# Kernel tuning notes

Measured on AMD Instinct MI355X. Metric: run time of the kernel, lower is better.

The kernel has to match this reference:

```python
import jax, jax.numpy as jnp
import numpy as np

N_CLASSES = 64
TRANSDUCTIVE_STEPS = 5


def setup_inputs() -> dict:
    key = jax.random.key(0)
    k1, k2, k3, k4 = jax.random.split(key, 4)
    support = jax.random.normal(k1, (1280, 2048), dtype=jnp.float32)
    query = jax.random.normal(k2, (65536, 2048), dtype=jnp.float32)
    support_labels = jax.random.randint(k3, (1280,), 0, N_CLASSES)
    W_enc = jax.random.normal(k4, (2048, 1024), dtype=jnp.float32) * 0.02
    b_enc = jnp.zeros((1024,), dtype=jnp.float32)
    return {"support": support, "query": query, "support_labels": support_labels,
            "W_enc": W_enc, "b_enc": b_enc}


def _segment_mean(emb, labels, n_seg):
    # masked-mean per class; empty classes stay zero (sum=0 / 1)
    sums = jax.ops.segment_sum(emb, labels, num_segments=n_seg)
    counts = jax.ops.segment_sum(jnp.ones((emb.shape[0],), emb.dtype), labels,
                                 num_segments=n_seg)
    return sums / jnp.maximum(counts, 1.0)[:, None]


def _cdist(x, p):
    # euclidean distance [n, d] x [c, d] -> [n, c]
    d2 = (jnp.sum(x * x, -1)[:, None] + jnp.sum(p * p, -1)[None, :]
          - 2.0 * x @ p.T)
    return jnp.sqrt(jnp.maximum(d2, 1e-12))


def reference(support, query, support_labels, W_enc, b_enc):
    support_emb = support @ W_enc + b_enc   # [ns, d]
    query_emb = query @ W_enc + b_enc       # [nq, d]

    prototypes = _segment_mean(support_emb, support_labels, N_CLASSES)
    all_emb = jnp.concatenate([support_emb, query_emb], axis=0)
    for _ in range(TRANSDUCTIVE_STEPS):
        query_labels = jnp.argmin(_cdist(query_emb, prototypes), axis=-1)
        all_labels = jnp.concatenate([support_labels, query_labels], axis=0)
        prototypes = _segment_mean(all_emb, all_labels, N_CLASSES)

    logits = -_cdist(query_emb, prototypes)  # [nq, n_classes]
    return logits
```

## Files before the change

kernel.cpp:

```cpp
#include <hip/hip_runtime.h>
#include <hip/hip_bf16.h>

#define NS 1280
#define NQ 65536
#define NA (NS + NQ)
#define DIN 2048
#define DEMB 1024
#define NC 64
#define STEPS 5
#define NDBLK (NQ / 128)

typedef __attribute__((ext_vector_type(8))) __bf16 bf16x8;
typedef __attribute__((ext_vector_type(4))) float f32x4;
typedef unsigned short u16;

__device__ __forceinline__ float b2f(u16 u) {
  return __uint_as_float(((unsigned int)u) << 16);
}
__device__ __forceinline__ u16 f2b(float f) {
  __hip_bfloat16 h = __float2bfloat16(f);
  u16 u; __builtin_memcpy(&u, &h, 2); return u;
}
__device__ __forceinline__ void gld_lds16(const void* g, void* l) {
  __builtin_amdgcn_global_load_lds(
      (const __attribute__((address_space(1))) void*)g,
      (__attribute__((address_space(3))) void*)l, 16, 0, 0);
}

__global__ __launch_bounds__(256) void cvt_bf16(const float4* __restrict__ in,
                                                ushort4* __restrict__ out, int n4) {
  for (int i = blockIdx.x * 256 + threadIdx.x; i < n4; i += gridDim.x * 256) {
    float4 v = in[i];
    ushort4 o;
    o.x = f2b(v.x); o.y = f2b(v.y); o.z = f2b(v.z); o.w = f2b(v.w);
    out[i] = o;
  }
}

__global__ __launch_bounds__(256) void transpose_w(const float* __restrict__ W,
                                                   u16* __restrict__ Wt) {
  __shared__ float tile[32][33];
  const int bx = blockIdx.x;
  const int by = blockIdx.y;
  const int tx = threadIdx.x & 31, ty = threadIdx.x >> 5;
#pragma unroll
  for (int j = 0; j < 4; j++)
    tile[ty + 8 * j][tx] = W[(size_t)(by * 32 + ty + 8 * j) * DEMB + bx * 32 + tx];
  __syncthreads();
#pragma unroll
  for (int j = 0; j < 4; j++)
    Wt[(size_t)(bx * 32 + ty + 8 * j) * DIN + by * 32 + tx] = f2b(tile[tx][ty + 8 * j]);
}

__device__ __forceinline__ void mm16(const bf16x8 af[4], const bf16x8 bf[4],
                                     f32x4 (&acc)[4][4]) {
#pragma unroll
  for (int mt = 0; mt < 4; ++mt)
#pragma unroll
    for (int nt = 0; nt < 4; ++nt)
      acc[mt][nt] = __builtin_amdgcn_mfma_f32_16x16x32_bf16(af[mt], bf[nt],
                                                            acc[mt][nt], 0, 0, 0);
}

__global__ __launch_bounds__(512, 2) void encoder_gemm(const u16* __restrict__ A,
                                                       const u16* __restrict__ Bt,
                                                       const float* __restrict__ bias,
                                                       u16* __restrict__ C) {
  const int b = blockIdx.x;
  const int x = b & 7, tt = b >> 3;
  const int mblk = x + 8 * (tt >> 2);
  const int nblk = tt & 3;
  if (mblk >= NA / 256) return;

  __shared__ u16 lds[65536];

  const int m0 = mblk * 256, n0 = nblk * 256;
  const int t = threadIdx.x;
  const int w = t >> 6, l = t & 63;
  const int wm = (w >> 2) * 128;
  const int wn = (w & 3) * 64;
  const int lr = l & 15, lk8 = (l >> 4) * 8;
  const int swz = (lr & 7) << 3;

  const int c1 = t + 512;
  const int r0 = t >> 3, r1 = c1 >> 3;
  const int sc0 = (((t & 7) ^ (r0 & 7)) << 3);
  const int sc1 = (((c1 & 7) ^ (r1 & 7)) << 3);

  const u16* gAt = A + (size_t)m0 * DIN;
  const u16* gBt = Bt + (size_t)n0 * DIN;

  f32x4 acc[2][4][4];
  f32x4 z; z.x = 0.f; z.y = 0.f; z.z = 0.f; z.w = 0.f;
#pragma unroll
  for (int g = 0; g < 2; ++g)
#pragma unroll
    for (int i = 0; i < 4; ++i)
#pragma unroll
      for (int j = 0; j < 4; ++j) acc[g][i][j] = z;

  auto STAGE = [&](const u16* g, u16* S, int h, int kb) {
    gld_lds16(g + (size_t)(h * 128 + r0) * DIN + kb + sc0, S + h * 8192 + t * 8);
    gld_lds16(g + (size_t)(h * 128 + r1) * DIN + kb + sc1, S + h * 8192 + c1 * 8);
  };

  STAGE(gAt, lds, 0, 0);
  STAGE(gAt, lds, 1, 0);
  STAGE(gBt, lds + 16384, 0, 0);
  STAGE(gBt, lds + 16384, 1, 0);

  const int NT = DIN / 64;
  for (int tk = 0; tk < NT; ++tk) {
    const int p = tk & 1;
    u16* LA = lds + p * 32768;
    u16* LB = LA + 16384;
    u16* SA = lds + (p ^ 1) * 32768;
    u16* SB = SA + 16384;
    const int kbn = (tk + 1) * 64;
    const bool pre = (tk + 1 < NT);

    bf16x8 af[4], bf0[4], bf1[4];

    if (pre) {
      STAGE(gAt, SA, 0, kbn);
      asm volatile("s_waitcnt vmcnt(2)" ::: "memory");
    } else {
      asm volatile("s_waitcnt vmcnt(0)" ::: "memory");
    }
    __builtin_amdgcn_s_barrier();
#pragma unroll
    for (int mt = 0; mt < 4; ++mt)
      af[mt] = *(const bf16x8*)&LA[(wm + mt * 16 + lr) * 64 + (lk8 ^ swz)];
#pragma unroll
    for (int nt = 0; nt < 4; ++nt)
      bf0[nt] = *(const bf16x8*)&LB[(wn + nt * 16 + lr) * 64 + (lk8 ^ swz)];
    __builtin_amdgcn_s_setprio(1);
    mm16(af, bf0, acc[0]);
    __builtin_amdgcn_s_setprio(0);
    __builtin_amdgcn_s_barrier();

#pragma unroll
    for (int mt = 0; mt < 4; ++mt)
      af[mt] = *(const bf16x8*)&LA[(wm + 64 + mt * 16 + lr) * 64 + (lk8 ^ swz)];
    if (pre) STAGE(gAt, SA, 1, kbn);
    __builtin_amdgcn_s_barrier();
    __builtin_amdgcn_s_setprio(1);
    mm16(af, bf0, acc[1]);
    __builtin_amdgcn_s_setprio(0);
    __builtin_amdgcn_s_barrier();

#pragma unroll
    for (int mt = 0; mt < 4; ++mt)
      af[mt] = *(const bf16x8*)&LA[(wm + mt * 16 + lr) * 64 + ((32 + lk8) ^ swz)];
#pragma unroll
    for (int nt = 0; nt < 4; ++nt)
      bf1[nt] = *(const bf16x8*)&LB[(wn + nt * 16 + lr) * 64 + ((32 + lk8) ^ swz)];
    if (pre) STAGE(gBt, SB, 0, kbn);
    __builtin_amdgcn_s_barrier();
    __builtin_amdgcn_s_setprio(1);
    mm16(af, bf1, acc[0]);
    __builtin_amdgcn_s_setprio(0);
    __builtin_amdgcn_s_barrier();

#pragma unroll
    for (int mt = 0; mt < 4; ++mt)
      af[mt] = *(const bf16x8*)&LA[(wm + 64 + mt * 16 + lr) * 64 + ((32 + lk8) ^ swz)];
    if (pre) STAGE(gBt, SB, 1, kbn);
    __builtin_amdgcn_s_barrier();
    __builtin_amdgcn_s_setprio(1);
    mm16(af, bf1, acc[1]);
    __builtin_amdgcn_s_setprio(0);
    __builtin_amdgcn_s_barrier();
  }

  float bv[4];
#pragma unroll
  for (int nt = 0; nt < 4; ++nt) bv[nt] = bias[n0 + wn + nt * 16 + lr];
#pragma unroll
  for (int mg = 0; mg < 2; ++mg)
#pragma unroll
    for (int mt = 0; mt < 4; ++mt)
#pragma unroll
      for (int nt = 0; nt < 4; ++nt)
#pragma unroll
        for (int r = 0; r < 4; ++r) {
          int row = m0 + wm + mg * 64 + mt * 16 + (l >> 4) * 4 + r;
          int col = n0 + wn + nt * 16 + lr;
          C[(size_t)row * DEMB + col] = f2b(acc[mg][mt][nt][r] + bv[nt]);
        }
}

__global__ __launch_bounds__(256) void support_sums(const u16* __restrict__ emb,
                                                    const int* __restrict__ slab,
                                                    float* __restrict__ ssum,
                                                    int* __restrict__ scount) {
  const int c = blockIdx.x, t = threadIdx.x;
  __shared__ int lab[NS];
  for (int i = t; i < NS; i += 256) lab[i] = slab[i];
  __syncthreads();
  float a0 = 0, a1 = 0, a2 = 0, a3 = 0;
  int cnt = 0;
  for (int i = 0; i < NS; i++) {
    if (lab[i] == c) {
      ushort4 e = *(const ushort4*)&emb[(size_t)i * DEMB + t * 4];
      a0 += b2f(e.x); a1 += b2f(e.y); a2 += b2f(e.z); a3 += b2f(e.w);
      cnt++;
    }
  }
  float* dst = ssum + (size_t)c * DEMB + t * 4;
  dst[0] = a0; dst[1] = a1; dst[2] = a2; dst[3] = a3;
  if (t == 0) scount[c] = cnt;
}

__global__ __launch_bounds__(256) void qnorm_kernel(const u16* __restrict__ Q,
                                                    float* __restrict__ qnorm) {
  const int t = threadIdx.x, w = t >> 6, l = t & 63;
  const int row = blockIdx.x * 4 + w;
  const u16* p = Q + (size_t)row * DEMB;
  float s = 0.f;
#pragma unroll
  for (int kk = 0; kk < 4; kk++) {
    ushort4 e = *(const ushort4*)&p[kk * 256 + l * 4];
    float x0 = b2f(e.x), x1 = b2f(e.y), x2 = b2f(e.z), x3 = b2f(e.w);
    s += x0 * x0 + x1 * x1 + x2 * x2 + x3 * x3;
  }
#pragma unroll
  for (int d = 32; d >= 1; d >>= 1) s += __shfl_xor(s, d);
  if (l == 0) qnorm[row] = s;
}

template <bool INIT>
__global__ __launch_bounds__(256) void finalize_protos(const float* __restrict__ ssum,
                                                       const int* __restrict__ scount,
                                                       const float* __restrict__ qpart,
                                                       const int* __restrict__ histpart,
                                                       u16* __restrict__ protos,
                                                       float* __restrict__ pnorm) {
  const int c = blockIdx.x, t = threadIdx.x;
  __shared__ int wredi[4];
  __shared__ float wredf[4];
  __shared__ int cnt_sh;
  float inv;
  if (INIT) {
    inv = 1.0f / fmaxf((float)scount[c], 1.0f);
  } else {
    int p = histpart[(size_t)c * NDBLK + t] + histpart[(size_t)c * NDBLK + 256 + t];
#pragma unroll
    for (int d = 32; d >= 1; d >>= 1) p += __shfl_xor(p, d);
    if ((t & 63) == 0) wredi[t >> 6] = p;
    __syncthreads();
    if (t == 0) cnt_sh = scount[c] + wredi[0] + wredi[1] + wredi[2] + wredi[3];
    __syncthreads();
    inv = 1.0f / fmaxf((float)cnt_sh, 1.0f);
  }
  float part = 0.f;
#pragma unroll
  for (int j = 0; j < 4; j++) {
    const int d = t * 4 + j;
    float v = ssum[(size_t)c * DEMB + d];
    if (!INIT) {
#pragma unroll
      for (int ch = 0; ch < 8; ch++)
        v += qpart[((size_t)ch * NC + c) * DEMB + d];
    }
    v *= inv;
    u16 bits = f2b(v);
    protos[(size_t)c * DEMB + d] = bits;
    float vb = b2f(bits);
    part += vb * vb;
  }
#pragma unroll
  for (int d = 32; d >= 1; d >>= 1) part += __shfl_xor(part, d);
  if ((t & 63) == 0) wredf[t >> 6] = part;
  __syncthreads();
  if (t == 0) pnorm[c] = wredf[0] + wredf[1] + wredf[2] + wredf[3];
}

template <int MODE>
__global__ __launch_bounds__(256) void dist_kernel(const u16* __restrict__ Q,
                                                   const u16* __restrict__ P,
                                                   const float* __restrict__ pnorm,
                                                   const float* __restrict__ qnorm,
                                                   int* __restrict__ labels,
                                                   int* __restrict__ histpart,
                                                   float* __restrict__ out) {
  __shared__ u16 As[128 * 32];
  __shared__ u16 Bs[64 * 32];
  __shared__ int hist[NC];
  const int t = threadIdx.x;
  if (MODE == 0 && t < NC) hist[t] = 0;
  const int m0 = blockIdx.x * 128;
  const int w = t >> 6, l = t & 63;
  const int lr = l & 15, lk = (l >> 4) * 8;
  const int wm = w * 32;

  f32x4 acc[2][4];
  f32x4 z; z.x = 0.f; z.y = 0.f; z.z = 0.f; z.w = 0.f;
#pragma unroll
  for (int i = 0; i < 2; i++)
#pragma unroll
    for (int j = 0; j < 4; j++) acc[i][j] = z;

  const int rA0 = t >> 2, k8 = (t & 3) * 8;
  const u16* gA = Q + (size_t)(m0 + rA0) * DEMB + k8;
  const u16* gB = P + (size_t)rA0 * DEMB + k8;
  u16* lA = As + t * 8;
  u16* lB = Bs + t * 8;

  for (int kb = 0; kb < DEMB; kb += 32) {
    gld_lds16(gA + kb, lA);
    gld_lds16(gA + kb + (size_t)64 * DEMB, lA + 64 * 32);
    gld_lds16(gB + kb, lB);
    __syncthreads();
    bf16x8 af[2], bf[4];
#pragma unroll
    for (int mt = 0; mt < 2; mt++) af[mt] = *(const bf16x8*)&As[(wm + mt * 16 + lr) * 32 + lk];
#pragma unroll
    for (int nt = 0; nt < 4; nt++) bf[nt] = *(const bf16x8*)&Bs[(nt * 16 + lr) * 32 + lk];
#pragma unroll
    for (int mt = 0; mt < 2; mt++)
#pragma unroll
      for (int nt = 0; nt < 4; nt++)
        acc[mt][nt] = __builtin_amdgcn_mfma_f32_16x16x32_bf16(af[mt], bf[nt], acc[mt][nt], 0, 0, 0);
    __syncthreads();
  }

  if (MODE == 0) {
#pragma unroll
    for (int mt = 0; mt < 2; mt++)
#pragma unroll
      for (int r = 0; r < 4; r++) {
        float best = 3.402e38f; int bc = 0;
#pragma unroll
        for (int nt = 0; nt < 4; nt++) {
          int col = nt * 16 + lr;
          float v = pnorm[col] - 2.0f * acc[mt][nt][r];
          if (v < best) { best = v; bc = col; }
        }
#pragma unroll
        for (int s = 1; s < 16; s <<= 1) {
          float ov = __shfl_xor(best, s);
          int oc = __shfl_xor(bc, s);
          if (ov < best || (ov == best && oc < bc)) { best = ov; bc = oc; }
        }
        if (lr == 0) {
          int row = m0 + wm + mt * 16 + (l >> 4) * 4 + r;
          labels[row] = bc;
          atomicAdd(&hist[bc], 1);
        }
      }
    __syncthreads();
    if (t < NC) histpart[(size_t)t * NDBLK + blockIdx.x] = hist[t];
  } else {
#pragma unroll
    for (int mt = 0; mt < 2; mt++)
#pragma unroll
      for (int nt = 0; nt < 4; nt++)
#pragma unroll
        for (int r = 0; r < 4; r++) {
          int row = m0 + wm + mt * 16 + (l >> 4) * 4 + r;
          int col = nt * 16 + lr;
          float d2 = qnorm[row] + pnorm[col] - 2.0f * acc[mt][nt][r];
          out[(size_t)row * NC + col] = -sqrtf(fmaxf(d2, 1e-12f));
        }
  }
}

__global__ __launch_bounds__(256) void class_gather_sum(const u16* __restrict__ Q,
                                                        const int* __restrict__ labels,
                                                        float* __restrict__ qpart) {
  const int c = blockIdx.x >> 3;
  const int chunk = blockIdx.x & 7;
  const int base = chunk * (NQ / 8);
  const int t = threadIdx.x;
  __shared__ int list[NQ / 8];
  __shared__ int nmatch;
  if (t == 0) nmatch = 0;
  __syncthreads();
  for (int i = t; i < NQ / 8; i += 256) {
    if (labels[base + i] == c) {
      int p = atomicAdd(&nmatch, 1);
      list[p] = base + i;
    }
  }
  __syncthreads();
  const int cnt = nmatch;
  float a0 = 0, a1 = 0, a2 = 0, a3 = 0;
  for (int j = 0; j < cnt; j++) {
    int row = list[j];
    ushort4 e = *(const ushort4*)&Q[(size_t)row * DEMB + t * 4];
    a0 += b2f(e.x); a1 += b2f(e.y); a2 += b2f(e.z); a3 += b2f(e.w);
  }
  float* dst = qpart + ((size_t)chunk * NC + c) * DEMB + t * 4;
  dst[0] = a0; dst[1] = a1; dst[2] = a2; dst[3] = a3;
}

extern "C" void kernel_launch(void* const* d_in, const int* in_sizes, int n_in,
                              void* d_out, int out_size, void* d_ws, size_t ws_size,
                              hipStream_t stream) {
  const float* support = (const float*)d_in[0];
  const float* query   = (const float*)d_in[1];
  const int*   slab    = (const int*)d_in[2];
  const float* W       = (const float*)d_in[3];
  const float* bias    = (const float*)d_in[4];
  float* out = (float*)d_out;

  u16* Abf = (u16*)d_ws;
  u16* Wt  = Abf + (size_t)NA * DIN;
  u16* emb = Wt + (size_t)DEMB * DIN;
  float* ssum  = (float*)(emb + (size_t)NA * DEMB);
  float* pnorm = ssum + (size_t)NC * DEMB;
  float* qnorm = pnorm + NC;
  int* scount  = (int*)(qnorm + NQ);
  int* labels  = scount + NC;
  u16* protos  = (u16*)(labels + NQ);
  float* qpart = (float*)Abf;
  int* histpart = (int*)(qpart + (size_t)8 * NC * DEMB);

  const u16* Qemb = emb + (size_t)NS * DEMB;

  cvt_bf16<<<2048, 256, 0, stream>>>((const float4*)support, (ushort4*)Abf,
                                     NS * DIN / 4);
  cvt_bf16<<<8192, 256, 0, stream>>>((const float4*)query,
                                     (ushort4*)(Abf + (size_t)NS * DIN),
                                     NQ * DIN / 4);
  transpose_w<<<dim3(32, 64), 256, 0, stream>>>(W, Wt);

  encoder_gemm<<<8 * 33 * 4, 512, 0, stream>>>(Abf, Wt, bias, emb);

  support_sums<<<NC, 256, 0, stream>>>(emb, slab, ssum, scount);
  qnorm_kernel<<<NQ / 4, 256, 0, stream>>>(Qemb, qnorm);

  finalize_protos<true><<<NC, 256, 0, stream>>>(ssum, scount, qpart, histpart,
                                                protos, pnorm);

  for (int it = 0; it < STEPS; ++it) {
    dist_kernel<0><<<NDBLK, 256, 0, stream>>>(Qemb, protos, pnorm, nullptr,
                                              labels, histpart, nullptr);
    class_gather_sum<<<NC * 8, 256, 0, stream>>>(Qemb, labels, qpart);
    finalize_protos<false><<<NC, 256, 0, stream>>>(ssum, scount, qpart, histpart,
                                                   protos, pnorm);
  }

  dist_kernel<1><<<NDBLK, 256, 0, stream>>>(Qemb, protos, pnorm, qnorm,
                                            nullptr, nullptr, out);
}
```

Before: 1.440 ms.

## Double-buffer dist kernel with swizzled 64-wide K tiles and issue GEMM prefetch upfront

```diff
diff --git a/kernel.cpp b/kernel.cpp
--- a/kernel.cpp
+++ b/kernel.cpp
@@ -123,7 +123,10 @@
 
     if (pre) {
       STAGE(gAt, SA, 0, kbn);
-      asm volatile("s_waitcnt vmcnt(2)" ::: "memory");
+      STAGE(gAt, SA, 1, kbn);
+      STAGE(gBt, SB, 0, kbn);
+      STAGE(gBt, SB, 1, kbn);
+      asm volatile("s_waitcnt vmcnt(8)" ::: "memory");
     } else {
       asm volatile("s_waitcnt vmcnt(0)" ::: "memory");
     }
@@ -142,7 +145,6 @@
 #pragma unroll
     for (int mt = 0; mt < 4; ++mt)
       af[mt] = *(const bf16x8*)&LA[(wm + 64 + mt * 16 + lr) * 64 + (lk8 ^ swz)];
-    if (pre) STAGE(gAt, SA, 1, kbn);
     __builtin_amdgcn_s_barrier();
     __builtin_amdgcn_s_setprio(1);
     mm16(af, bf0, acc[1]);
@@ -155,7 +157,6 @@
 #pragma unroll
     for (int nt = 0; nt < 4; ++nt)
       bf1[nt] = *(const bf16x8*)&LB[(wn + nt * 16 + lr) * 64 + ((32 + lk8) ^ swz)];
-    if (pre) STAGE(gBt, SB, 0, kbn);
     __builtin_amdgcn_s_barrier();
     __builtin_amdgcn_s_setprio(1);
     mm16(af, bf1, acc[0]);
@@ -165,7 +166,6 @@
 #pragma unroll
     for (int mt = 0; mt < 4; ++mt)
       af[mt] = *(const bf16x8*)&LA[(wm + 64 + mt * 16 + lr) * 64 + ((32 + lk8) ^ swz)];
-    if (pre) STAGE(gBt, SB, 1, kbn);
     __builtin_amdgcn_s_barrier();
     __builtin_amdgcn_s_setprio(1);
     mm16(af, bf1, acc[1]);
@@ -284,15 +284,16 @@
                                                    int* __restrict__ labels,
                                                    int* __restrict__ histpart,
                                                    float* __restrict__ out) {
-  __shared__ u16 As[128 * 32];
-  __shared__ u16 Bs[64 * 32];
+  __shared__ __align__(16) u16 Ab[2][128 * 64];
+  __shared__ __align__(16) u16 Bb[2][64 * 64];
   __shared__ int hist[NC];
   const int t = threadIdx.x;
   if (MODE == 0 && t < NC) hist[t] = 0;
   const int m0 = blockIdx.x * 128;
   const int w = t >> 6, l = t & 63;
-  const int lr = l & 15, lk = (l >> 4) * 8;
+  const int lr = l & 15, lk8 = (l >> 4) * 8;
   const int wm = w * 32;
+  const int swz = (lr & 7) << 3;
 
   f32x4 acc[2][4];
   f32x4 z; z.x = 0.f; z.y = 0.f; z.z = 0.f; z.w = 0.f;
@@ -301,28 +302,59 @@
 #pragma unroll
     for (int j = 0; j < 4; j++) acc[i][j] = z;
 
-  const int rA0 = t >> 2, k8 = (t & 3) * 8;
-  const u16* gA = Q + (size_t)(m0 + rA0) * DEMB + k8;
-  const u16* gB = P + (size_t)rA0 * DEMB + k8;
-  u16* lA = As + t * 8;
-  u16* lB = Bs + t * 8;
-
-  for (int kb = 0; kb < DEMB; kb += 32) {
-    gld_lds16(gA + kb, lA);
-    gld_lds16(gA + kb + (size_t)64 * DEMB, lA + 64 * 32);
-    gld_lds16(gB + kb, lB);
-    __syncthreads();
-    bf16x8 af[2], bf[4];
-#pragma unroll
-    for (int mt = 0; mt < 2; mt++) af[mt] = *(const bf16x8*)&As[(wm + mt * 16 + lr) * 32 + lk];
-#pragma unroll
-    for (int nt = 0; nt < 4; nt++) bf[nt] = *(const bf16x8*)&Bs[(nt * 16 + lr) * 32 + lk];
-#pragma unroll
-    for (int mt = 0; mt < 2; mt++)
-#pragma unroll
-      for (int nt = 0; nt < 4; nt++)
-        acc[mt][nt] = __builtin_amdgcn_mfma_f32_16x16x32_bf16(af[mt], bf[nt], acc[mt][nt], 0, 0, 0);
-    __syncthreads();
+  int rA[4], sA[4], rB[2], sB[2];
+#pragma unroll
+  for (int j = 0; j < 4; ++j) {
+    int c = t + 256 * j;
+    rA[j] = c >> 3;
+    sA[j] = ((c & 7) ^ (rA[j] & 7)) << 3;
+  }
+#pragma unroll
+  for (int j = 0; j < 2; ++j) {
+    int c = t + 256 * j;
+    rB[j] = c >> 3;
+    sB[j] = ((c & 7) ^ (rB[j] & 7)) << 3;
+  }
+
+  auto STAGE = [&](int buf, int kb) {
+#pragma unroll
+    for (int j = 0; j < 4; ++j)
+      gld_lds16(Q + (size_t)(m0 + rA[j]) * DEMB + kb + sA[j], &Ab[buf][(t + 256 * j) * 8]);
+#pragma unroll
+    for (int j = 0; j < 2; ++j)
+      gld_lds16(P + (size_t)rB[j] * DEMB + kb + sB[j], &Bb[buf][(t + 256 * j) * 8]);
+  };
+
+  STAGE(0, 0);
+  const int NT = DEMB / 64;
+  for (int tk = 0; tk < NT; ++tk) {
+    const int cur = tk & 1;
+    if (tk + 1 < NT) {
+      STAGE(cur ^ 1, (tk + 1) * 64);
+      asm volatile("s_waitcnt vmcnt(6)" ::: "memory");
+    } else {
+      asm volatile("s_waitcnt vmcnt(0)" ::: "memory");
+    }
+    __builtin_amdgcn_s_barrier();
+    bf16x8 af[2][2], bf[2][4];
+#pragma unroll
+    for (int kk = 0; kk < 2; ++kk) {
+#pragma unroll
+      for (int mt = 0; mt < 2; ++mt)
+        af[kk][mt] = *(const bf16x8*)&Ab[cur][(wm + mt * 16 + lr) * 64 + ((kk * 32 + lk8) ^ swz)];
+#pragma unroll
+      for (int nt = 0; nt < 4; ++nt)
+        bf[kk][nt] = *(const bf16x8*)&Bb[cur][(nt * 16 + lr) * 64 + ((kk * 32 + lk8) ^ swz)];
+    }
+#pragma unroll
+    for (int kk = 0; kk < 2; ++kk)
+#pragma unroll
+      for (int mt = 0; mt < 2; ++mt)
+#pragma unroll
+        for (int nt = 0; nt < 4; ++nt)
+          acc[mt][nt] = __builtin_amdgcn_mfma_f32_16x16x32_bf16(af[kk][mt], bf[kk][nt],
+                                                                acc[mt][nt], 0, 0, 0);
+    __builtin_amdgcn_s_barrier();
   }
 
   if (MODE == 0) {
```

Measured after the change: 1.513 ms. +5.0%, slower.

## Rework GEMM prefetch schedule and make dist kernel load operands directly from global

Applied to the files above, without the earlier changes.

```diff
diff --git a/kernel.cpp b/kernel.cpp
--- a/kernel.cpp
+++ b/kernel.cpp
@@ -8,7 +8,7 @@
 #define DEMB 1024
 #define NC 64
 #define STEPS 5
-#define NDBLK (NQ / 128)
+#define NDBLK (NQ / 64)
 
 typedef __attribute__((ext_vector_type(8))) __bf16 bf16x8;
 typedef __attribute__((ext_vector_type(4))) float f32x4;
@@ -108,6 +108,8 @@
   STAGE(gAt, lds, 1, 0);
   STAGE(gBt, lds + 16384, 0, 0);
   STAGE(gBt, lds + 16384, 1, 0);
+  asm volatile("s_waitcnt vmcnt(0)" ::: "memory");
+  __builtin_amdgcn_s_barrier();
 
   const int NT = DIN / 64;
   for (int tk = 0; tk < NT; ++tk) {
@@ -121,29 +123,28 @@
 
     bf16x8 af[4], bf0[4], bf1[4];
 
-    if (pre) {
-      STAGE(gAt, SA, 0, kbn);
-      asm volatile("s_waitcnt vmcnt(2)" ::: "memory");
-    } else {
-      asm volatile("s_waitcnt vmcnt(0)" ::: "memory");
-    }
-    __builtin_amdgcn_s_barrier();
+    if (pre) { STAGE(gAt, SA, 0, kbn); STAGE(gAt, SA, 1, kbn); }
 #pragma unroll
     for (int mt = 0; mt < 4; ++mt)
       af[mt] = *(const bf16x8*)&LA[(wm + mt * 16 + lr) * 64 + (lk8 ^ swz)];
 #pragma unroll
     for (int nt = 0; nt < 4; ++nt)
       bf0[nt] = *(const bf16x8*)&LB[(wn + nt * 16 + lr) * 64 + (lk8 ^ swz)];
+    __builtin_amdgcn_s_barrier();
+    asm volatile("s_waitcnt lgkmcnt(0)" ::: "memory");
+    __builtin_amdgcn_sched_barrier(0);
     __builtin_amdgcn_s_setprio(1);
     mm16(af, bf0, acc[0]);
     __builtin_amdgcn_s_setprio(0);
     __builtin_amdgcn_s_barrier();
 
+    if (pre) { STAGE(gBt, SB, 0, kbn); STAGE(gBt, SB, 1, kbn); }
 #pragma unroll
     for (int mt = 0; mt < 4; ++mt)
       af[mt] = *(const bf16x8*)&LA[(wm + 64 + mt * 16 + lr) * 64 + (lk8 ^ swz)];
-    if (pre) STAGE(gAt, SA, 1, kbn);
-    __builtin_amdgcn_s_barrier();
+    __builtin_amdgcn_s_barrier();
+    asm volatile("s_waitcnt lgkmcnt(0)" ::: "memory");
+    __builtin_amdgcn_sched_barrier(0);
     __builtin_amdgcn_s_setprio(1);
     mm16(af, bf0, acc[1]);
     __builtin_amdgcn_s_setprio(0);
@@ -155,8 +156,10 @@
 #pragma unroll
     for (int nt = 0; nt < 4; ++nt)
       bf1[nt] = *(const bf16x8*)&LB[(wn + nt * 16 + lr) * 64 + ((32 + lk8) ^ swz)];
-    if (pre) STAGE(gBt, SB, 0, kbn);
-    __builtin_amdgcn_s_barrier();
+    if (pre) asm volatile("s_waitcnt vmcnt(4)" ::: "memory");
+    __builtin_amdgcn_s_barrier();
+    asm volatile("s_waitcnt lgkmcnt(0)" ::: "memory");
+    __builtin_amdgcn_sched_barrier(0);
     __builtin_amdgcn_s_setprio(1);
     mm16(af, bf1, acc[0]);
     __builtin_amdgcn_s_setprio(0);
@@ -165,8 +168,10 @@
 #pragma unroll
     for (int mt = 0; mt < 4; ++mt)
       af[mt] = *(const bf16x8*)&LA[(wm + 64 + mt * 16 + lr) * 64 + ((32 + lk8) ^ swz)];
-    if (pre) STAGE(gBt, SB, 1, kbn);
-    __builtin_amdgcn_s_barrier();
+    if (pre) asm volatile("s_waitcnt vmcnt(0)" ::: "memory");
+    __builtin_amdgcn_s_barrier();
+    asm volatile("s_waitcnt lgkmcnt(0)" ::: "memory");
+    __builtin_amdgcn_sched_barrier(0);
     __builtin_amdgcn_s_setprio(1);
     mm16(af, bf1, acc[1]);
     __builtin_amdgcn_s_setprio(0);
@@ -244,7 +249,8 @@
   if (INIT) {
     inv = 1.0f / fmaxf((float)scount[c], 1.0f);
   } else {
-    int p = histpart[(size_t)c * NDBLK + t] + histpart[(size_t)c * NDBLK + 256 + t];
+    int p = histpart[(size_t)c * NDBLK + t] + histpart[(size_t)c * NDBLK + 256 + t]
+          + histpart[(size_t)c * NDBLK + 512 + t] + histpart[(size_t)c * NDBLK + 768 + t];
 #pragma unroll
     for (int d = 32; d >= 1; d >>= 1) p += __shfl_xor(p, d);
     if ((t & 63) == 0) wredi[t >> 6] = p;
@@ -284,85 +290,78 @@
                                                    int* __restrict__ labels,
                                                    int* __restrict__ histpart,
                                                    float* __restrict__ out) {
-  __shared__ u16 As[128 * 32];
-  __shared__ u16 Bs[64 * 32];
   __shared__ int hist[NC];
   const int t = threadIdx.x;
-  if (MODE == 0 && t < NC) hist[t] = 0;
-  const int m0 = blockIdx.x * 128;
+  if (MODE == 0) {
+    if (t < NC) hist[t] = 0;
+    __syncthreads();
+  }
   const int w = t >> 6, l = t & 63;
-  const int lr = l & 15, lk = (l >> 4) * 8;
-  const int wm = w * 32;
-
-  f32x4 acc[2][4];
+  const int lr = l & 15, lk8 = (l >> 4) * 8;
+  const int row16 = blockIdx.x * 64 + w * 16;
+  const u16* qrow = Q + (size_t)(row16 + lr) * DEMB + lk8;
+  const u16* prow = P + (size_t)lr * DEMB + lk8;
+
+  f32x4 acc[4];
   f32x4 z; z.x = 0.f; z.y = 0.f; z.z = 0.f; z.w = 0.f;
 #pragma unroll
-  for (int i = 0; i < 2; i++)
-#pragma unroll
-    for (int j = 0; j < 4; j++) acc[i][j] = z;
-
-  const int rA0 = t >> 2, k8 = (t & 3) * 8;
-  const u16* gA = Q + (size_t)(m0 + rA0) * DEMB + k8;
-  const u16* gB = P + (size_t)rA0 * DEMB + k8;
-  u16* lA = As + t * 8;
-  u16* lB = Bs + t * 8;
-
-  for (int kb = 0; kb < DEMB; kb += 32) {
-    gld_lds16(gA + kb, lA);
-    gld_lds16(gA + kb + (size_t)64 * DEMB, lA + 64 * 32);
-    gld_lds16(gB + kb, lB);
-    __syncthreads();
-    bf16x8 af[2], bf[4];
-#pragma unroll
-    for (int mt = 0; mt < 2; mt++) af[mt] = *(const bf16x8*)&As[(wm + mt * 16 + lr) * 32 + lk];
-#pragma unroll
-    for (int nt = 0; nt < 4; nt++) bf[nt] = *(const bf16x8*)&Bs[(nt * 16 + lr) * 32 + lk];
-#pragma unroll
-    for (int mt = 0; mt < 2; mt++)
-#pragma unroll
-      for (int nt = 0; nt < 4; nt++)
-        acc[mt][nt] = __builtin_amdgcn_mfma_f32_16x16x32_bf16(af[mt], bf[nt], acc[mt][nt], 0, 0, 0);
-    __syncthreads();
+  for (int j = 0; j < 4; j++) acc[j] = z;
+
+  bf16x8 a0 = *(const bf16x8*)&qrow[0];
+  bf16x8 a1 = *(const bf16x8*)&qrow[32];
+  for (int kb = 0; kb < DEMB; kb += 64) {
+    bf16x8 c0 = a0, c1 = a1;
+    if (kb + 64 < DEMB) {
+      a0 = *(const bf16x8*)&qrow[kb + 64];
+      a1 = *(const bf16x8*)&qrow[kb + 96];
+    }
+    bf16x8 b0[4], b1[4];
+#pragma unroll
+    for (int nt = 0; nt < 4; ++nt) {
+      b0[nt] = *(const bf16x8*)&prow[(size_t)nt * 16 * DEMB + kb];
+      b1[nt] = *(const bf16x8*)&prow[(size_t)nt * 16 * DEMB + kb + 32];
+    }
+#pragma unroll
+    for (int nt = 0; nt < 4; ++nt) {
+      acc[nt] = __builtin_amdgcn_mfma_f32_16x16x32_bf16(c0, b0[nt], acc[nt], 0, 0, 0);
+      acc[nt] = __builtin_amdgcn_mfma_f32_16x16x32_bf16(c1, b1[nt], acc[nt], 0, 0, 0);
+    }
   }
 
   if (MODE == 0) {
 #pragma unroll
-    for (int mt = 0; mt < 2; mt++)
-#pragma unroll
-      for (int r = 0; r < 4; r++) {
-        float best = 3.402e38f; int bc = 0;
-#pragma unroll
-        for (int nt = 0; nt < 4; nt++) {
-          int col = nt * 16 + lr;
-          float v = pnorm[col] - 2.0f * acc[mt][nt][r];
-          if (v < best) { best = v; bc = col; }
-        }
-#pragma unroll
-        for (int s = 1; s < 16; s <<= 1) {
-          float ov = __shfl_xor(best, s);
-          int oc = __shfl_xor(bc, s);
-          if (ov < best || (ov == best && oc < bc)) { best = ov; bc = oc; }
-        }
-        if (lr == 0) {
-          int row = m0 + wm + mt * 16 + (l >> 4) * 4 + r;
-          labels[row] = bc;
-          atomicAdd(&hist[bc], 1);
-        }
+    for (int r = 0; r < 4; r++) {
+      float best = 3.402e38f; int bc = 0;
+#pragma unroll
+      for (int nt = 0; nt < 4; nt++) {
+        int col = nt * 16 + lr;
+        float v = pnorm[col] - 2.0f * acc[nt][r];
+        if (v < best) { best = v; bc = col; }
       }
+#pragma unroll
+      for (int s = 1; s < 16; s <<= 1) {
+        float ov = __shfl_xor(best, s);
+        int oc = __shfl_xor(bc, s);
+        if (ov < best || (ov == best && oc < bc)) { best = ov; bc = oc; }
+      }
+      if (lr == 0) {
+        int row = row16 + (l >> 4) * 4 + r;
+        labels[row] = bc;
+        atomicAdd(&hist[bc], 1);
+      }
+    }
     __syncthreads();
     if (t < NC) histpart[(size_t)t * NDBLK + blockIdx.x] = hist[t];
   } else {
 #pragma unroll
-    for (int mt = 0; mt < 2; mt++)
-#pragma unroll
-      for (int nt = 0; nt < 4; nt++)
-#pragma unroll
-        for (int r = 0; r < 4; r++) {
-          int row = m0 + wm + mt * 16 + (l >> 4) * 4 + r;
-          int col = nt * 16 + lr;
-          float d2 = qnorm[row] + pnorm[col] - 2.0f * acc[mt][nt][r];
-          out[(size_t)row * NC + col] = -sqrtf(fmaxf(d2, 1e-12f));
-        }
+    for (int nt = 0; nt < 4; nt++)
+#pragma unroll
+      for (int r = 0; r < 4; r++) {
+        int row = row16 + (l >> 4) * 4 + r;
+        int col = nt * 16 + lr;
+        float d2 = qnorm[row] + pnorm[col] - 2.0f * acc[nt][r];
+        out[(size_t)row * NC + col] = -sqrtf(fmaxf(d2, 1e-12f));
+      }
   }
 }
 
```

New measurement: 1.770 ms. 1.23x slower.
